# Kernel optimization log

Hardware: AMD Instinct MI355X
Metric: run time of the kernel (lower is better)

The kernel has to match this reference:

```python
import jax, jax.numpy as jnp
import numpy as np

D_STATE = 16; D_MODEL = 256; N_HEADS = 8; N_LAYERS = 4; D_REL = 64
HEALTH = 0
WORLD = (1024.0, 1024.0)
B, T, N = 32, 512, 8
ACTION_DIM = 12


def setup_inputs() -> dict:
    key = jax.random.key(0)
    ks = iter(jax.random.split(key, 48))
    s = 0.02
    def w(shape):
        return jax.random.normal(next(ks), shape, jnp.float32) * s
    inp = dict(
        state=jax.random.normal(next(ks), (B, T, N, D_STATE), jnp.float32),
        pos=jax.random.uniform(next(ks), (B, T, N, 2), jnp.float32),
        vel=jax.random.normal(next(ks), (B, T, N, 2), jnp.float32),
        team_ids=jax.random.randint(next(ks), (B, T, N), 0, 2, jnp.int32),
        alive=jax.random.randint(next(ks), (B, T, N), 0, 2, jnp.int32).astype(bool),
        dead=jnp.zeros((D_STATE,), jnp.float32),
        enc_W1=w((D_STATE, D_MODEL)), enc_b1=jnp.zeros((D_MODEL,), jnp.float32),
        enc_W2=w((D_MODEL, D_MODEL)), enc_b2=jnp.zeros((D_MODEL,), jnp.float32),
        team_emb=w((2, D_MODEL)), ship_emb=w((8, D_MODEL)),
        trunk_W1=w((6, D_REL)), trunk_b1=jnp.zeros((D_REL,), jnp.float32),
        trunk_W2=w((D_REL, D_REL)), trunk_b2=jnp.zeros((D_REL,), jnp.float32),
        adapt_W=w((N_LAYERS, D_REL, N_HEADS)), adapt_b=jnp.zeros((N_LAYERS, N_HEADS), jnp.float32),
        norm_w=jnp.ones((N_LAYERS, D_MODEL), jnp.float32),
        Wq=w((N_LAYERS, D_MODEL, D_MODEL)), bq=jnp.zeros((N_LAYERS, D_MODEL), jnp.float32),
        Wk=w((N_LAYERS, D_MODEL, D_MODEL)), bk=jnp.zeros((N_LAYERS, D_MODEL), jnp.float32),
        Wv=w((N_LAYERS, D_MODEL, D_MODEL)), bv=jnp.zeros((N_LAYERS, D_MODEL), jnp.float32),
        Wo=w((N_LAYERS, D_MODEL, D_MODEL)), bo=jnp.zeros((N_LAYERS, D_MODEL), jnp.float32),
        head_W=w((D_MODEL, ACTION_DIM)), head_b=jnp.zeros((ACTION_DIM,), jnp.float32),
    )
    return inp


def _rms(x, g, eps=1e-6):
    return x * jax.lax.rsqrt(jnp.mean(x * x, axis=-1, keepdims=True) + eps) * g


def reference(state, pos, vel, team_ids, alive, dead,
              enc_W1, enc_b1, enc_W2, enc_b2, team_emb, ship_emb,
              trunk_W1, trunk_b1, trunk_W2, trunk_b2, adapt_W, adapt_b,
              norm_w, Wq, bq, Wk, bk, Wv, bv, Wo, bo, head_W, head_b):
    ws = jnp.asarray(WORLD, state.dtype)
    # replace dead entities' state with learned 'dead' vector
    state = jnp.where(alive[..., None], state, dead)
    # state encoder (MLP)
    h = jax.nn.silu(state @ enc_W1 + enc_b1) @ enc_W2 + enc_b2
    # special embeddings
    h = h + team_emb[team_ids] + ship_emb[jnp.arange(N)]  # ship_emb broadcasts over B,T
    # relational trunk: pairwise toroidal geometry features [B,T,N,N,6]
    p = pos * ws
    rel = p[:, :, :, None, :] - p[:, :, None, :, :]
    rel = rel - jnp.round(rel / ws) * ws  # toroidal wrap
    relv = vel[:, :, :, None, :] - vel[:, :, None, :, :]
    dn = jnp.sqrt(jnp.sum(rel * rel, axis=-1) + 1e-8) / ws[0]
    feats = jnp.concatenate([rel / ws, relv, dn[..., None], 1.0 / (1.0 + dn[..., None])], axis=-1)
    trunk = jax.nn.silu(feats @ trunk_W1 + trunk_b1) @ trunk_W2 + trunk_b2  # [B,T,N,N,D_REL]
    dh = D_MODEL // N_HEADS
    scale = dh ** -0.5
    kmask = alive[:, :, None, None, :]  # mask keys
    x = h
    for i in range(N_LAYERS):
        nx = _rms(x, norm_w[i])
        # adapter: per-layer relational bias [B,T,H,N,N]
        bias = jnp.transpose(trunk @ adapt_W[i] + adapt_b[i], (0, 1, 4, 2, 3))
        q = (nx @ Wq[i] + bq[i]).reshape(B, T, N, N_HEADS, dh)
        k = (nx @ Wk[i] + bk[i]).reshape(B, T, N, N_HEADS, dh)
        v = (nx @ Wv[i] + bv[i]).reshape(B, T, N, N_HEADS, dh)
        sc = jnp.einsum('btihd,btjhd->bthij', q, k) * scale + bias
        sc = jnp.where(kmask, sc, -1e9)
        a = jax.nn.softmax(sc, axis=-1)
        o = jnp.einsum('bthij,btjhd->btihd', a, v).reshape(B, T, N, D_MODEL)
        x = x + o @ Wo[i] + bo[i]
    action_logits = x @ head_W + head_b  # [B,T,N,12]
    return action_logits
```

## Files before the change

kernel.cpp:

```cpp
#include <hip/hip_runtime.h>
#include <cstdint>

#define DEV __device__ __forceinline__

typedef __attribute__((ext_vector_type(8))) short short8;
typedef __attribute__((ext_vector_type(4))) float floatx4;
typedef unsigned short u16;
typedef unsigned int u32;

DEV u16 f2bf(float f) {
    unsigned u = __float_as_uint(f);
    return (u16)((u + 0x7fffu + ((u >> 16) & 1u)) >> 16);
}
DEV void unpack2(u32 u, float& a, float& b) {
    a = __uint_as_float(u << 16);
    b = __uint_as_float(u & 0xffff0000u);
}
DEV u32 pack2f(float a, float b) { return (u32)f2bf(a) | ((u32)f2bf(b) << 16); }
DEV float sigm(float x) { return 1.0f / (1.0f + __expf(-x)); }

#define NAG 8
#define DM 256
#define NL 4
#define AD 12
#define MROWS 32
#define NBLK 4096

#define OFF_E1   0
#define OFF_E2   8192
#define OFF_QKVO 73728
#define OFF_TW2  1122304
#define OFF_ADW  1126400
#define WS_TOTAL 1128448
#define WS_BYTES (WS_TOTAL * 2)

#define L_R1    0
#define L_KB    16896
#define L_V     33792
#define L_R2    50688
#define L_RED   67584
#define L_SPOS  68096
#define L_SVEL  68352
#define SMEM_BYTES 68608

#define TRK(row, col) ((row) * 64 + ((((col) >> 3) ^ ((row) & 7)) << 3) + ((col) & 7))

enum { I_STATE=0, I_POS, I_VEL, I_TEAM, I_ALIVE, I_DEAD, I_EW1, I_EB1, I_EW2, I_EB2,
       I_TEMB, I_SEMB, I_TW1, I_TB1, I_TW2, I_TB2, I_ADW, I_ADB, I_NORMW,
       I_WQ, I_BQ, I_WK, I_BK, I_WV, I_BV, I_WO, I_BO, I_HW, I_HB, N_IN };

struct Args { const void* in[N_IN]; float* out; };

__global__ __launch_bounds__(256) void prep_kernel(Args a, u16* ws)
{
    int e = blockIdx.x * 256 + threadIdx.x;
    int mat = blockIdx.y;
    int size, offs, N, Kreal;
    const float* src;
    if (mat == 0)      { size = 8192;  offs = OFF_E1;  N = 256; Kreal = 16;  src = (const float*)a.in[I_EW1]; }
    else if (mat == 1) { size = 65536; offs = OFF_E2;  N = 256; Kreal = 256; src = (const float*)a.in[I_EW2]; }
    else if (mat < 18) {
        int q = mat - 2, l = q >> 2, m = q & 3;
        int wi = (m == 0) ? I_WQ : (m == 1) ? I_WK : (m == 2) ? I_WV : I_WO;
        size = 65536; offs = OFF_QKVO + q * 65536; N = 256; Kreal = 256;
        src = (const float*)a.in[wi] + l * 65536;
    }
    else if (mat == 18) { size = 4096; offs = OFF_TW2; N = 64; Kreal = 64; src = (const float*)a.in[I_TW2]; }
    else                { size = 2048; offs = OFF_ADW; N = 32; Kreal = 64; src = (const float*)a.in[I_ADW]; }
    if (e >= size) return;
    int ksblk = N * 32;
    int ks = e / ksblk, rem = e % ksblk;
    int n = rem >> 5, quad = (rem >> 3) & 3, j = rem & 7;
    int k = ks * 32 + quad * 8 + j;
    float v = 0.0f;
    if (k < Kreal) {
        if (mat == 19) v = src[((n >> 3) * 64 + k) * 8 + (n & 7)];
        else           v = src[k * N + n];
    }
    ws[offs + e] = f2bf(v);
}

DEV short8 ld_u4(const u16* p) {
    return __builtin_bit_cast(short8, *(const uint4*)p);
}
DEV short8 ld_afrag(const u16* A, int stride, int row0, int kofs, int l15, int quad) {
    return ld_u4(A + (row0 + l15) * stride + kofs + quad * 8);
}
DEV short8 ld_bws(const u16* w, int ksblk, int ks, int col, int l15, int quad) {
    return ld_u4(w + ks * ksblk + (col + l15) * 32 + quad * 8);
}
DEV short8 ld_bf32(const float* W, int N, int Kreal, int ks, int col, int l15, int quad) {
    short8 r;
    #pragma unroll
    for (int j = 0; j < 8; j++) {
        int k = ks * 32 + quad * 8 + j;
        float v = (k < Kreal) ? W[k * N + col + l15] : 0.0f;
        r[j] = (short)f2bf(v);
    }
    return r;
}

template<bool UW>
DEV void gemm32(const u16* A, const u16* wsW, const float* Wf,
                int Kb, int Kreal, int colw, int l15, int quad, floatx4 acc[2][4]) {
    for (int ks = 0; ks < Kb; ks++) {
        short8 af0 = ld_afrag(A, 264, 0,  ks * 32, l15, quad);
        short8 af1 = ld_afrag(A, 264, 16, ks * 32, l15, quad);
        short8 bf[4];
        #pragma unroll
        for (int nj = 0; nj < 4; nj++)
            bf[nj] = UW ? ld_bws(wsW, 8192, ks, colw + nj * 16, l15, quad)
                        : ld_bf32(Wf, 256, Kreal, ks, colw + nj * 16, l15, quad);
        #pragma unroll
        for (int nj = 0; nj < 4; nj++) {
            acc[0][nj] = __builtin_amdgcn_mfma_f32_16x16x32_bf16(af0, bf[nj], acc[0][nj], 0, 0, 0);
            acc[1][nj] = __builtin_amdgcn_mfma_f32_16x16x32_bf16(af1, bf[nj], acc[1][nj], 0, 0, 0);
        }
    }
}

template<bool UW>
__global__ __launch_bounds__(256, 2) void yemong_mfma(Args a, const u16* ws)
{
    extern __shared__ char smem[];
    u16* sR1   = (u16*)(smem + L_R1);
    u16* skb   = (u16*)(smem + L_KB);
    u16* sV    = (u16*)(smem + L_V);
    u16* sR2   = (u16*)(smem + L_R2);
    float* sred = (float*)(smem + L_RED);
    float* spos = (float*)(smem + L_SPOS);
    float* svel = (float*)(smem + L_SVEL);

    const int t = threadIdx.x, bid = blockIdx.x;
    const int lane = t & 63, w = t >> 6;
    const int l15 = lane & 15, quad = lane >> 4;
    const int colw = w * 64;
    const int p = w >> 1, h0 = (w & 1) * 4;

    float xr[2][4][4];
    u32 br[NL][4][2];
    u32 amask;

    unsigned mp = 0;
    const unsigned* au = (const unsigned*)a.in[I_ALIVE];
    #pragma unroll
    for (int i = 0; i < 16; i++) mp |= au[i];
    const bool abyte = (mp > 1u);
    auto aliveAt = [&](int r) -> int {
        int gi = bid * MROWS + r;
        return abyte ? (int)((const unsigned char*)a.in[I_ALIVE])[gi]
                     : ((const int*)a.in[I_ALIVE])[gi];
    };
    auto rms_partials = [&]() {
        float ssv[8];
        #pragma unroll
        for (int mi = 0; mi < 2; mi++)
            #pragma unroll
            for (int r = 0; r < 4; r++) {
                float s = 0.0f;
                #pragma unroll
                for (int nj = 0; nj < 4; nj++) { float v = xr[mi][nj][r]; s = fmaf(v, v, s); }
                ssv[mi * 4 + r] = s;
            }
        #pragma unroll
        for (int m = 1; m < 16; m <<= 1)
            #pragma unroll
            for (int k2 = 0; k2 < 8; k2++) ssv[k2] += __shfl_xor(ssv[k2], m);
        if (l15 == 0) {
            #pragma unroll
            for (int mi = 0; mi < 2; mi++)
                #pragma unroll
                for (int r = 0; r < 4; r++)
                    sred[(mi * 16 + quad * 4 + r) * 4 + w] = ssv[mi * 4 + r];
        }
    };

    if (t < 64) {
        int n = t >> 1, d = t & 1;
        spos[n * 2 + d] = ((const float*)a.in[I_POS])[(bid * MROWS + n) * 2 + d] * 1024.0f;
        svel[n * 2 + d] = ((const float*)a.in[I_VEL])[(bid * MROWS + n) * 2 + d];
    }
    {
        int tk = 2 * p + (quad >> 1);
        amask = 0;
        #pragma unroll
        for (int j = 0; j < 8; j++) amask |= (aliveAt(tk * 8 + j) ? 1u : 0u) << j;
    }
    {
        const float* gs = (const float*)a.in[I_STATE];
        const float* gd = (const float*)a.in[I_DEAD];
        #pragma unroll
        for (int it = 0; it < 4; it++) {
            int idx = t + 256 * it;
            int r = idx >> 5, kk = idx & 31;
            float v = 0.0f;
            if (kk < 16) v = aliveAt(r) ? gs[(bid * MROWS + r) * 16 + kk] : gd[kk];
            sR2[r * 264 + kk] = f2bf(v);
        }
    }
    __syncthreads();

    {
        floatx4 acc[2][4] = {};
        gemm32<UW>(sR2, ws + OFF_E1, (const float*)a.in[I_EW1], 1, 16, colw, l15, quad, acc);
        __syncthreads();
        const float* b1 = (const float*)a.in[I_EB1];
        #pragma unroll
        for (int nj = 0; nj < 4; nj++) {
            int c = colw + nj * 16 + l15;
            float bb = b1[c];
            #pragma unroll
            for (int mi = 0; mi < 2; mi++)
                #pragma unroll
                for (int r = 0; r < 4; r++) {
                    float v = acc[mi][nj][r] + bb;
                    sR2[(mi * 16 + quad * 4 + r) * 264 + c] = f2bf(v * sigm(v));
                }
        }
    }
    __syncthreads();

    {
        floatx4 acc[2][4] = {};
        gemm32<UW>(sR2, ws + OFF_E2, (const float*)a.in[I_EW2], 8, 256, colw, l15, quad, acc);
        const float* b2 = (const float*)a.in[I_EB2];
        const float* te = (const float*)a.in[I_TEMB];
        const float* se = (const float*)a.in[I_SEMB];
        const int* gteam = (const int*)a.in[I_TEAM];
        int team8[8];
        #pragma unroll
        for (int mi = 0; mi < 2; mi++)
            #pragma unroll
            for (int r = 0; r < 4; r++)
                team8[mi * 4 + r] = gteam[bid * MROWS + mi * 16 + quad * 4 + r];
        #pragma unroll
        for (int nj = 0; nj < 4; nj++) {
            int c = colw + nj * 16 + l15;
            float bb = b2[c];
            #pragma unroll
            for (int mi = 0; mi < 2; mi++)
                #pragma unroll
                for (int r = 0; r < 4; r++) {
                    int row = mi * 16 + quad * 4 + r;
                    xr[mi][nj][r] = acc[mi][nj][r] + bb + te[team8[mi * 4 + r] * 256 + c] + se[(row & 7) * 256 + c];
                }
        }
        rms_partials();
    }

    {
        int tokp = t >> 6;
        int pi = tokp * 8 + ((t >> 3) & 7), pj = tokp * 8 + (t & 7);
        float rx = spos[pi * 2 + 0] - spos[pj * 2 + 0];
        float ry = spos[pi * 2 + 1] - spos[pj * 2 + 1];
        rx -= rintf(rx * (1.0f / 1024.0f)) * 1024.0f;
        ry -= rintf(ry * (1.0f / 1024.0f)) * 1024.0f;
        float vx = svel[pi * 2 + 0] - svel[pj * 2 + 0];
        float vy = svel[pi * 2 + 1] - svel[pj * 2 + 1];
        float dn = sqrtf(rx * rx + ry * ry + 1e-8f) * (1.0f / 1024.0f);
        float f[6] = {rx * (1.0f / 1024.0f), ry * (1.0f / 1024.0f), vx, vy, dn, 1.0f / (1.0f + dn)};
        const float* W1 = (const float*)a.in[I_TW1];
        const float* B1 = (const float*)a.in[I_TB1];
        #pragma unroll
        for (int g = 0; g < 8; g++) {
            float v[8];
            #pragma unroll
            for (int e = 0; e < 8; e++) v[e] = B1[g * 8 + e];
            #pragma unroll
            for (int kk = 0; kk < 6; kk++)
                #pragma unroll
                for (int e = 0; e < 8; e++) v[e] = fmaf(f[kk], W1[kk * 64 + g * 8 + e], v[e]);
            #pragma unroll
            for (int e = 0; e < 8; e++) v[e] = v[e] * sigm(v[e]);
            uint4 pk;
            pk.x = pack2f(v[0], v[1]); pk.y = pack2f(v[2], v[3]);
            pk.z = pack2f(v[4], v[5]); pk.w = pack2f(v[6], v[7]);
            *(uint4*)&sR1[t * 64 + ((g ^ (t & 7)) << 3)] = pk;
        }
    }
    __syncthreads();

    {
        short8 taf[4][2];
        #pragma unroll
        for (int mi = 0; mi < 4; mi++)
            #pragma unroll
            for (int ks = 0; ks < 2; ks++) {
                int R = colw + mi * 16 + l15;
                taf[mi][ks] = ld_u4(&sR1[R * 64 + (((ks * 4 + quad) ^ (R & 7)) << 3)]);
            }
        floatx4 tacc[4][4] = {};
        #pragma unroll
        for (int ks = 0; ks < 2; ks++) {
            short8 bf[4];
            #pragma unroll
            for (int nj = 0; nj < 4; nj++)
                bf[nj] = UW ? ld_bws(ws + OFF_TW2, 2048, ks, nj * 16, l15, quad)
                            : ld_bf32((const float*)a.in[I_TW2], 64, 64, ks, nj * 16, l15, quad);
            #pragma unroll
            for (int mi = 0; mi < 4; mi++)
                #pragma unroll
                for (int nj = 0; nj < 4; nj++)
                    tacc[mi][nj] = __builtin_amdgcn_mfma_f32_16x16x32_bf16(taf[mi][ks], bf[nj], tacc[mi][nj], 0, 0, 0);
        }
        const float* B2 = (const float*)a.in[I_TB2];
        #pragma unroll
        for (int nj = 0; nj < 4; nj++) {
            int c = nj * 16 + l15;
            float bb = B2[c];
            #pragma unroll
            for (int mi = 0; mi < 4; mi++)
                #pragma unroll
                for (int r = 0; r < 4; r++) {
                    int row = colw + mi * 16 + quad * 4 + r;
                    sR1[TRK(row, c)] = f2bf(tacc[mi][nj][r] + bb);
                }
        }
    }
    __syncthreads();

    {
        floatx4 tacc[4][2] = {};
        #pragma unroll
        for (int ks = 0; ks < 2; ks++) {
            short8 bf[2];
            #pragma unroll
            for (int nj = 0; nj < 2; nj++) {
                if (UW) bf[nj] = ld_bws(ws + OFF_ADW, 1024, ks, nj * 16, l15, quad);
                else {
                    const float* adw = (const float*)a.in[I_ADW];
                    int n = nj * 16 + l15;
                    #pragma unroll
                    for (int j = 0; j < 8; j++) {
                        int k = ks * 32 + quad * 8 + j;
                        bf[nj][j] = (short)f2bf(k < 64 ? adw[((n >> 3) * 64 + k) * 8 + (n & 7)] : 0.0f);
                    }
                }
            }
            #pragma unroll
            for (int mi = 0; mi < 4; mi++) {
                int R = colw + mi * 16 + l15;
                short8 af = ld_u4(&sR1[R * 64 + (((ks * 4 + quad) ^ (R & 7)) << 3)]);
                #pragma unroll
                for (int nj = 0; nj < 2; nj++)
                    tacc[mi][nj] = __builtin_amdgcn_mfma_f32_16x16x32_bf16(af, bf[nj], tacc[mi][nj], 0, 0, 0);
            }
        }
        const float* adb = (const float*)a.in[I_ADB];
        #pragma unroll
        for (int nj = 0; nj < 2; nj++) {
            int n = nj * 16 + l15;
            float bb = adb[n];
            #pragma unroll
            for (int mi = 0; mi < 4; mi++)
                #pragma unroll
                for (int r = 0; r < 4; r++) {
                    int pl = mi * 16 + quad * 4 + r;
                    sR2[((w * 4 + (n >> 3)) * 8 + (n & 7)) * 64 + pl] = f2bf(tacc[mi][nj][r] + bb);
                }
        }
        __syncthreads();
        int tk = 2 * p + (quad >> 1);
        #pragma unroll
        for (int l = 0; l < NL; l++)
            #pragma unroll
            for (int u = 0; u < 4; u++) {
                int base = ((tk * 4 + l) * 8 + (h0 + u)) * 64 + (l15 & 7) * 8 + (quad & 1) * 4;
                const u32* bp = (const u32*)&sR2[base];
                br[l][u][0] = bp[0];
                br[l][u][1] = bp[1];
            }
    }
    __syncthreads();

    const float* normw = (const float*)a.in[I_NORMW];
    const bool qvalid = ((quad >> 1) == (l15 >> 3));
    #pragma unroll
    for (int l = 0; l < NL; l++) {
        {
            float invr[8];
            #pragma unroll
            for (int mi = 0; mi < 2; mi++)
                #pragma unroll
                for (int r = 0; r < 4; r++) {
                    int row = mi * 16 + quad * 4 + r;
                    float s = sred[row * 4 + 0] + sred[row * 4 + 1] + sred[row * 4 + 2] + sred[row * 4 + 3];
                    invr[mi * 4 + r] = rsqrtf(s * (1.0f / 256.0f) + 1e-6f);
                }
            #pragma unroll
            for (int nj = 0; nj < 4; nj++) {
                int c = colw + nj * 16 + l15;
                float nwv = normw[l * 256 + c];
                #pragma unroll
                for (int mi = 0; mi < 2; mi++)
                    #pragma unroll
                    for (int r = 0; r < 4; r++)
                        sR2[(mi * 16 + quad * 4 + r) * 264 + c] = f2bf(xr[mi][nj][r] * invr[mi * 4 + r] * nwv);
            }
        }
        __syncthreads();

        {
            floatx4 acc[3][2][4] = {};
            const u16* wq  = ws + OFF_QKVO + (l * 4 + 0) * 65536;
            const u16* wk  = ws + OFF_QKVO + (l * 4 + 1) * 65536;
            const u16* wvv = ws + OFF_QKVO + (l * 4 + 2) * 65536;
            const float* fq = (const float*)a.in[I_WQ] + l * 65536;
            const float* fk = (const float*)a.in[I_WK] + l * 65536;
            const float* fv = (const float*)a.in[I_WV] + l * 65536;
            #pragma unroll 2
            for (int ks = 0; ks < 8; ks++) {
                short8 af0 = ld_afrag(sR2, 264, 0,  ks * 32, l15, quad);
                short8 af1 = ld_afrag(sR2, 264, 16, ks * 32, l15, quad);
                short8 bq[4], bk[4], bv[4];
                #pragma unroll
                for (int nj = 0; nj < 4; nj++) {
                    int c = colw + nj * 16;
                    bq[nj] = UW ? ld_bws(wq,  8192, ks, c, l15, quad) : ld_bf32(fq, 256, 256, ks, c, l15, quad);
                    bk[nj] = UW ? ld_bws(wk,  8192, ks, c, l15, quad) : ld_bf32(fk, 256, 256, ks, c, l15, quad);
                    bv[nj] = UW ? ld_bws(wvv, 8192, ks, c, l15, quad) : ld_bf32(fv, 256, 256, ks, c, l15, quad);
                }
                #pragma unroll
                for (int nj = 0; nj < 4; nj++) {
                    acc[0][0][nj] = __builtin_amdgcn_mfma_f32_16x16x32_bf16(af0, bq[nj], acc[0][0][nj], 0, 0, 0);
                    acc[0][1][nj] = __builtin_amdgcn_mfma_f32_16x16x32_bf16(af1, bq[nj], acc[0][1][nj], 0, 0, 0);
                    acc[1][0][nj] = __builtin_amdgcn_mfma_f32_16x16x32_bf16(af0, bk[nj], acc[1][0][nj], 0, 0, 0);
                    acc[1][1][nj] = __builtin_amdgcn_mfma_f32_16x16x32_bf16(af1, bk[nj], acc[1][1][nj], 0, 0, 0);
                    acc[2][0][nj] = __builtin_amdgcn_mfma_f32_16x16x32_bf16(af0, bv[nj], acc[2][0][nj], 0, 0, 0);
                    acc[2][1][nj] = __builtin_amdgcn_mfma_f32_16x16x32_bf16(af1, bv[nj], acc[2][1][nj], 0, 0, 0);
                }
            }
            const float* bqf = (const float*)a.in[I_BQ] + l * 256;
            const float* bkf = (const float*)a.in[I_BK] + l * 256;
            const float* bvf = (const float*)a.in[I_BV] + l * 256;
            #pragma unroll
            for (int nj = 0; nj < 4; nj++) {
                int c = colw + nj * 16 + l15;
                float b0 = bqf[c], b1 = bkf[c], b2v = bvf[c];
                #pragma unroll
                for (int mi = 0; mi < 2; mi++)
                    #pragma unroll
                    for (int r = 0; r < 4; r++) {
                        int row = mi * 16 + quad * 4 + r;
                        sR1[row * 264 + c] = f2bf((acc[0][mi][nj][r] + b0) * 0.17677669529663689f);
                        skb[row * 264 + c] = f2bf(acc[1][mi][nj][r] + b1);
                        sV [row * 264 + c] = f2bf(acc[2][mi][nj][r] + b2v);
                    }
            }
        }
        __syncthreads();

        {
            short8 kf[4], qf[4];
            #pragma unroll
            for (int u = 0; u < 4; u++) {
                int h = h0 + u;
                kf[u] = ld_u4(&skb[(p * 16 + l15) * 264 + h * 32 + quad * 8]);
                qf[u] = ld_u4(&sR1[(p * 16 + l15) * 264 + h * 32 + quad * 8]);
            }
            floatx4 st[4];
            #pragma unroll
            for (int u = 0; u < 4; u++) {
                floatx4 zero = {};
                st[u] = __builtin_amdgcn_mfma_f32_16x16x32_bf16(kf[u], qf[u], zero, 0, 0, 0);
            }
            short8 paf[4];
            #pragma unroll
            for (int u = 0; u < 4; u++) {
                float bb[4];
                unpack2(br[l][u][0], bb[0], bb[1]);
                unpack2(br[l][u][1], bb[2], bb[3]);
                float s[4];
                #pragma unroll
                for (int r = 0; r < 4; r++) {
                    int jl = (quad & 1) * 4 + r;
                    bool alv = (amask >> jl) & 1;
                    s[r] = qvalid ? (alv ? st[u][r] + bb[r] : -1.0e9f) : -2.0e9f;
                }
                float mx = fmaxf(fmaxf(s[0], s[1]), fmaxf(s[2], s[3]));
                mx = fmaxf(mx, __shfl_xor(mx, 16));
                mx = fmaxf(mx, __shfl_xor(mx, 32));
                float e[4], sm = 0.0f;
                #pragma unroll
                for (int r = 0; r < 4; r++) { e[r] = __expf(s[r] - mx); sm += e[r]; }
                sm += __shfl_xor(sm, 16);
                sm += __shfl_xor(sm, 32);
                float inv = 1.0f / sm;
                u32 u01 = pack2f(e[0] * inv, e[1] * inv);
                u32 u23 = pack2f(e[2] * inv, e[3] * inv);
                int srcA = (quad * 32 + l15) & 63;
                u32 a0 = (u32)__shfl((int)u01, srcA);
                u32 a1 = (u32)__shfl((int)u23, srcA);
                u32 a2 = (u32)__shfl((int)u01, (srcA + 16) & 63);
                u32 a3 = (u32)__shfl((int)u23, (srcA + 16) & 63);
                if (quad >= 2) { a0 = 0; a1 = 0; a2 = 0; a3 = 0; }
                uint4 tmp; tmp.x = a0; tmp.y = a1; tmp.z = a2; tmp.w = a3;
                paf[u] = __builtin_bit_cast(short8, tmp);
            }
            #pragma unroll
            for (int u = 0; u < 4; u++) {
                int h = h0 + u;
                #pragma unroll
                for (int nt = 0; nt < 2; nt++) {
                    short8 vf;
                    if (quad < 2) {
                        #pragma unroll
                        for (int jj = 0; jj < 8; jj++) {
                            int kr = quad * 8 + jj;
                            vf[jj] = (short)sV[(p * 16 + kr) * 264 + h * 32 + nt * 16 + l15];
                        }
                    } else {
                        #pragma unroll
                        for (int jj = 0; jj < 8; jj++) vf[jj] = 0;
                    }
                    floatx4 z2 = {};
                    floatx4 o = __builtin_amdgcn_mfma_f32_16x16x32_bf16(paf[u], vf, z2, 0, 0, 0);
                    #pragma unroll
                    for (int r = 0; r < 4; r++)
                        sR1[(p * 16 + quad * 4 + r) * 264 + h * 32 + nt * 16 + l15] = f2bf(o[r]);
                }
            }
        }
        __syncthreads();

        {
            floatx4 acc[2][4] = {};
            gemm32<UW>(sR1, ws + OFF_QKVO + (l * 4 + 3) * 65536, (const float*)a.in[I_WO] + l * 65536,
                       8, 256, colw, l15, quad, acc);
            const float* bo = (const float*)a.in[I_BO] + l * 256;
            #pragma unroll
            for (int nj = 0; nj < 4; nj++) {
                float bb = bo[colw + nj * 16 + l15];
                #pragma unroll
                for (int mi = 0; mi < 2; mi++)
                    #pragma unroll
                    for (int r = 0; r < 4; r++)
                        xr[mi][nj][r] += acc[mi][nj][r] + bb;
            }
            rms_partials();
        }
        __syncthreads();
    }

    {
        float* xf = (float*)sR1;
        #pragma unroll
        for (int nj = 0; nj < 4; nj++) {
            int c = colw + nj * 16 + l15;
            #pragma unroll
            for (int mi = 0; mi < 2; mi++)
                #pragma unroll
                for (int r = 0; r < 4; r++)
                    xf[(mi * 16 + quad * 4 + r) * 264 + c] = xr[mi][nj][r];
        }
        __syncthreads();
        int row = t >> 3, pp = t & 7;
        const float* HW = (const float*)a.in[I_HW];
        float ah[12];
        #pragma unroll
        for (int c = 0; c < 12; c++) ah[c] = 0.0f;
        for (int kk = pp * 32; kk < pp * 32 + 32; kk++) {
            float xv = xf[row * 264 + kk];
            #pragma unroll
            for (int c = 0; c < 12; c++) ah[c] = fmaf(xv, HW[kk * 12 + c], ah[c]);
        }
        #pragma unroll
        for (int c = 0; c < 12; c++) {
            ah[c] += __shfl_xor(ah[c], 1);
            ah[c] += __shfl_xor(ah[c], 2);
            ah[c] += __shfl_xor(ah[c], 4);
        }
        if (pp == 0) {
            const float* hb = (const float*)a.in[I_HB];
            #pragma unroll
            for (int c = 0; c < 12; c++)
                a.out[(bid * MROWS + row) * AD + c] = ah[c] + hb[c];
        }
    }
}

extern "C" void kernel_launch(void* const* d_in, const int* in_sizes, int n_in,
                              void* d_out, int out_size, void* d_ws, size_t ws_size,
                              hipStream_t stream) {
    (void)in_sizes; (void)n_in; (void)out_size;
    Args a;
    for (int i = 0; i < N_IN; i++) a.in[i] = d_in[i];
    a.out = (float*)d_out;
    u16* ws16 = (u16*)d_ws;
    const bool use_ws = (ws_size >= (size_t)WS_BYTES) && (d_ws != nullptr);
    if (use_ws) {
        hipLaunchKernelGGL(prep_kernel, dim3(256, 20), dim3(256), 0, stream, a, ws16);
        hipFuncSetAttribute((const void*)yemong_mfma<true>, hipFuncAttributeMaxDynamicSharedMemorySize, SMEM_BYTES);
        hipLaunchKernelGGL((yemong_mfma<true>), dim3(NBLK), dim3(256), SMEM_BYTES, stream, a, ws16);
    } else {
        hipFuncSetAttribute((const void*)yemong_mfma<false>, hipFuncAttributeMaxDynamicSharedMemorySize, SMEM_BYTES);
        hipLaunchKernelGGL((yemong_mfma<false>), dim3(NBLK), dim3(256), SMEM_BYTES, stream, a, ws16);
    }
}
```

Baseline: 1.124 ms.

## Double rows per block to 64 with 512 threads and reshape GEMM warp tiling

```diff
diff --git a/kernel.cpp b/kernel.cpp
--- a/kernel.cpp
+++ b/kernel.cpp
@@ -23,8 +23,9 @@
 #define DM 256
 #define NL 4
 #define AD 12
-#define MROWS 32
-#define NBLK 4096
+#define MROWS 64
+#define NBLK 2048
+#define THREADS 512
 
 #define OFF_E1   0
 #define OFF_E2   8192
@@ -35,13 +36,13 @@
 #define WS_BYTES (WS_TOTAL * 2)
 
 #define L_R1    0
-#define L_KB    16896
-#define L_V     33792
-#define L_R2    50688
-#define L_RED   67584
-#define L_SPOS  68096
-#define L_SVEL  68352
-#define SMEM_BYTES 68608
+#define L_KB    33792
+#define L_V     67584
+#define L_R2    101376
+#define L_RED   135168
+#define L_SPOS  137216
+#define L_SVEL  137728
+#define SMEM_BYTES 138240
 
 #define TRK(row, col) ((row) * 64 + ((((col) >> 3) ^ ((row) & 7)) << 3) + ((col) & 7))
 
@@ -101,26 +102,29 @@
 }
 
 template<bool UW>
-DEV void gemm32(const u16* A, const u16* wsW, const float* Wf,
-                int Kb, int Kreal, int colw, int l15, int quad, floatx4 acc[2][4]) {
+DEV void gemm64(const u16* A, const u16* wsW, const float* Wf,
+                int Kb, int Kreal, int colw, int l15, int quad, floatx4 acc[4][2]) {
+    #pragma unroll 2
     for (int ks = 0; ks < Kb; ks++) {
-        short8 af0 = ld_afrag(A, 264, 0,  ks * 32, l15, quad);
-        short8 af1 = ld_afrag(A, 264, 16, ks * 32, l15, quad);
-        short8 bf[4];
-        #pragma unroll
-        for (int nj = 0; nj < 4; nj++)
+        short8 af[4];
+        #pragma unroll
+        for (int mi = 0; mi < 4; mi++)
+            af[mi] = ld_afrag(A, 264, mi * 16, ks * 32, l15, quad);
+        short8 bf[2];
+        #pragma unroll
+        for (int nj = 0; nj < 2; nj++)
             bf[nj] = UW ? ld_bws(wsW, 8192, ks, colw + nj * 16, l15, quad)
                         : ld_bf32(Wf, 256, Kreal, ks, colw + nj * 16, l15, quad);
         #pragma unroll
-        for (int nj = 0; nj < 4; nj++) {
-            acc[0][nj] = __builtin_amdgcn_mfma_f32_16x16x32_bf16(af0, bf[nj], acc[0][nj], 0, 0, 0);
-            acc[1][nj] = __builtin_amdgcn_mfma_f32_16x16x32_bf16(af1, bf[nj], acc[1][nj], 0, 0, 0);
-        }
+        for (int mi = 0; mi < 4; mi++)
+            #pragma unroll
+            for (int nj = 0; nj < 2; nj++)
+                acc[mi][nj] = __builtin_amdgcn_mfma_f32_16x16x32_bf16(af[mi], bf[nj], acc[mi][nj], 0, 0, 0);
     }
 }
 
 template<bool UW>
-__global__ __launch_bounds__(256, 2) void yemong_mfma(Args a, const u16* ws)
+__global__ __launch_bounds__(THREADS, 2) void yemong_mfma(Args a, const u16* ws)
 {
     extern __shared__ char smem[];
     u16* sR1   = (u16*)(smem + L_R1);
@@ -134,10 +138,11 @@
     const int t = threadIdx.x, bid = blockIdx.x;
     const int lane = t & 63, w = t >> 6;
     const int l15 = lane & 15, quad = lane >> 4;
-    const int colw = w * 64;
+    const int colw = w * 32;
+    const int rowt = w * 64;
     const int p = w >> 1, h0 = (w & 1) * 4;
 
-    float xr[2][4][4];
+    float xr[4][2][4];
     u32 br[NL][4][2];
     u32 amask;
 
@@ -152,30 +157,28 @@
                      : ((const int*)a.in[I_ALIVE])[gi];
     };
     auto rms_partials = [&]() {
-        float ssv[8];
-        #pragma unroll
-        for (int mi = 0; mi < 2; mi++)
+        float ssv[16];
+        #pragma unroll
+        for (int mi = 0; mi < 4; mi++)
             #pragma unroll
             for (int r = 0; r < 4; r++) {
-                float s = 0.0f;
-                #pragma unroll
-                for (int nj = 0; nj < 4; nj++) { float v = xr[mi][nj][r]; s = fmaf(v, v, s); }
-                ssv[mi * 4 + r] = s;
+                float x0 = xr[mi][0][r], x1 = xr[mi][1][r];
+                ssv[mi * 4 + r] = fmaf(x0, x0, x1 * x1);
             }
         #pragma unroll
         for (int m = 1; m < 16; m <<= 1)
             #pragma unroll
-            for (int k2 = 0; k2 < 8; k2++) ssv[k2] += __shfl_xor(ssv[k2], m);
+            for (int k2 = 0; k2 < 16; k2++) ssv[k2] += __shfl_xor(ssv[k2], m);
         if (l15 == 0) {
             #pragma unroll
-            for (int mi = 0; mi < 2; mi++)
+            for (int mi = 0; mi < 4; mi++)
                 #pragma unroll
                 for (int r = 0; r < 4; r++)
-                    sred[(mi * 16 + quad * 4 + r) * 4 + w] = ssv[mi * 4 + r];
+                    sred[(mi * 16 + quad * 4 + r) * 8 + w] = ssv[mi * 4 + r];
         }
     };
 
-    if (t < 64) {
+    if (t < 128) {
         int n = t >> 1, d = t & 1;
         spos[n * 2 + d] = ((const float*)a.in[I_POS])[(bid * MROWS + n) * 2 + d] * 1024.0f;
         svel[n * 2 + d] = ((const float*)a.in[I_VEL])[(bid * MROWS + n) * 2 + d];
@@ -191,7 +194,7 @@
         const float* gd = (const float*)a.in[I_DEAD];
         #pragma unroll
         for (int it = 0; it < 4; it++) {
-            int idx = t + 256 * it;
+            int idx = t + THREADS * it;
             int r = idx >> 5, kk = idx & 31;
             float v = 0.0f;
             if (kk < 16) v = aliveAt(r) ? gs[(bid * MROWS + r) * 16 + kk] : gd[kk];
@@ -201,16 +204,16 @@
     __syncthreads();
 
     {
-        floatx4 acc[2][4] = {};
-        gemm32<UW>(sR2, ws + OFF_E1, (const float*)a.in[I_EW1], 1, 16, colw, l15, quad, acc);
+        floatx4 acc[4][2] = {};
+        gemm64<UW>(sR2, ws + OFF_E1, (const float*)a.in[I_EW1], 1, 16, colw, l15, quad, acc);
         __syncthreads();
         const float* b1 = (const float*)a.in[I_EB1];
         #pragma unroll
-        for (int nj = 0; nj < 4; nj++) {
+        for (int nj = 0; nj < 2; nj++) {
             int c = colw + nj * 16 + l15;
             float bb = b1[c];
             #pragma unroll
-            for (int mi = 0; mi < 2; mi++)
+            for (int mi = 0; mi < 4; mi++)
                 #pragma unroll
                 for (int r = 0; r < 4; r++) {
                     float v = acc[mi][nj][r] + bb;
@@ -221,28 +224,28 @@
     __syncthreads();
 
     {
-        floatx4 acc[2][4] = {};
-        gemm32<UW>(sR2, ws + OFF_E2, (const float*)a.in[I_EW2], 8, 256, colw, l15, quad, acc);
+        floatx4 acc[4][2] = {};
+        gemm64<UW>(sR2, ws + OFF_E2, (const float*)a.in[I_EW2], 8, 256, colw, l15, quad, acc);
         const float* b2 = (const float*)a.in[I_EB2];
         const float* te = (const float*)a.in[I_TEMB];
         const float* se = (const float*)a.in[I_SEMB];
         const int* gteam = (const int*)a.in[I_TEAM];
-        int team8[8];
-        #pragma unroll
-        for (int mi = 0; mi < 2; mi++)
+        int team16[16];
+        #pragma unroll
+        for (int mi = 0; mi < 4; mi++)
             #pragma unroll
             for (int r = 0; r < 4; r++)
-                team8[mi * 4 + r] = gteam[bid * MROWS + mi * 16 + quad * 4 + r];
-        #pragma unroll
-        for (int nj = 0; nj < 4; nj++) {
+                team16[mi * 4 + r] = gteam[bid * MROWS + mi * 16 + quad * 4 + r];
+        #pragma unroll
+        for (int nj = 0; nj < 2; nj++) {
             int c = colw + nj * 16 + l15;
             float bb = b2[c];
             #pragma unroll
-            for (int mi = 0; mi < 2; mi++)
+            for (int mi = 0; mi < 4; mi++)
                 #pragma unroll
                 for (int r = 0; r < 4; r++) {
                     int row = mi * 16 + quad * 4 + r;
-                    xr[mi][nj][r] = acc[mi][nj][r] + bb + te[team8[mi * 4 + r] * 256 + c] + se[(row & 7) * 256 + c];
+                    xr[mi][nj][r] = acc[mi][nj][r] + bb + te[team16[mi * 4 + r] * 256 + c] + se[(row & 7) * 256 + c];
                 }
         }
         rms_partials();
@@ -286,7 +289,7 @@
         for (int mi = 0; mi < 4; mi++)
             #pragma unroll
             for (int ks = 0; ks < 2; ks++) {
-                int R = colw + mi * 16 + l15;
+                int R = rowt + mi * 16 + l15;
                 taf[mi][ks] = ld_u4(&sR1[R * 64 + (((ks * 4 + quad) ^ (R & 7)) << 3)]);
             }
         floatx4 tacc[4][4] = {};
@@ -312,7 +315,7 @@
             for (int mi = 0; mi < 4; mi++)
                 #pragma unroll
                 for (int r = 0; r < 4; r++) {
-                    int row = colw + mi * 16 + quad * 4 + r;
+                    int row = rowt + mi * 16 + quad * 4 + r;
                     sR1[TRK(row, c)] = f2bf(tacc[mi][nj][r] + bb);
                 }
         }
@@ -339,7 +342,7 @@
             }
             #pragma unroll
             for (int mi = 0; mi < 4; mi++) {
-                int R = colw + mi * 16 + l15;
+                int R = rowt + mi * 16 + l15;
                 short8 af = ld_u4(&sR1[R * 64 + (((ks * 4 + quad) ^ (R & 7)) << 3)]);
                 #pragma unroll
                 for (int nj = 0; nj < 2; nj++)
@@ -378,21 +381,23 @@
     #pragma unroll
     for (int l = 0; l < NL; l++) {
         {
-            float invr[8];
-            #pragma unroll
-            for (int mi = 0; mi < 2; mi++)
+            float invr[16];
+            #pragma unroll
+            for (int mi = 0; mi < 4; mi++)
                 #pragma unroll
                 for (int r = 0; r < 4; r++) {
                     int row = mi * 16 + quad * 4 + r;
-                    float s = sred[row * 4 + 0] + sred[row * 4 + 1] + sred[row * 4 + 2] + sred[row * 4 + 3];
+                    float4 pa = *(const float4*)&sred[row * 8];
+                    float4 pb = *(const float4*)&sred[row * 8 + 4];
+                    float s = pa.x + pa.y + pa.z + pa.w + pb.x + pb.y + pb.z + pb.w;
                     invr[mi * 4 + r] = rsqrtf(s * (1.0f / 256.0f) + 1e-6f);
                 }
             #pragma unroll
-            for (int nj = 0; nj < 4; nj++) {
+            for (int nj = 0; nj < 2; nj++) {
                 int c = colw + nj * 16 + l15;
                 float nwv = normw[l * 256 + c];
                 #pragma unroll
-                for (int mi = 0; mi < 2; mi++)
+                for (int mi = 0; mi < 4; mi++)
                     #pragma unroll
                     for (int r = 0; r < 4; r++)
                         sR2[(mi * 16 + quad * 4 + r) * 264 + c] = f2bf(xr[mi][nj][r] * invr[mi * 4 + r] * nwv);
@@ -401,51 +406,50 @@
         __syncthreads();
 
         {
-            floatx4 acc[3][2][4] = {};
-            const u16* wq  = ws + OFF_QKVO + (l * 4 + 0) * 65536;
-            const u16* wk  = ws + OFF_QKVO + (l * 4 + 1) * 65536;
-            const u16* wvv = ws + OFF_QKVO + (l * 4 + 2) * 65536;
-            const float* fq = (const float*)a.in[I_WQ] + l * 65536;
-            const float* fk = (const float*)a.in[I_WK] + l * 65536;
-            const float* fv = (const float*)a.in[I_WV] + l * 65536;
-            #pragma unroll 2
-            for (int ks = 0; ks < 8; ks++) {
-                short8 af0 = ld_afrag(sR2, 264, 0,  ks * 32, l15, quad);
-                short8 af1 = ld_afrag(sR2, 264, 16, ks * 32, l15, quad);
-                short8 bq[4], bk[4], bv[4];
-                #pragma unroll
-                for (int nj = 0; nj < 4; nj++) {
-                    int c = colw + nj * 16;
-                    bq[nj] = UW ? ld_bws(wq,  8192, ks, c, l15, quad) : ld_bf32(fq, 256, 256, ks, c, l15, quad);
-                    bk[nj] = UW ? ld_bws(wk,  8192, ks, c, l15, quad) : ld_bf32(fk, 256, 256, ks, c, l15, quad);
-                    bv[nj] = UW ? ld_bws(wvv, 8192, ks, c, l15, quad) : ld_bf32(fv, 256, 256, ks, c, l15, quad);
-                }
-                #pragma unroll
-                for (int nj = 0; nj < 4; nj++) {
-                    acc[0][0][nj] = __builtin_amdgcn_mfma_f32_16x16x32_bf16(af0, bq[nj], acc[0][0][nj], 0, 0, 0);
-                    acc[0][1][nj] = __builtin_amdgcn_mfma_f32_16x16x32_bf16(af1, bq[nj], acc[0][1][nj], 0, 0, 0);
-                    acc[1][0][nj] = __builtin_amdgcn_mfma_f32_16x16x32_bf16(af0, bk[nj], acc[1][0][nj], 0, 0, 0);
-                    acc[1][1][nj] = __builtin_amdgcn_mfma_f32_16x16x32_bf16(af1, bk[nj], acc[1][1][nj], 0, 0, 0);
-                    acc[2][0][nj] = __builtin_amdgcn_mfma_f32_16x16x32_bf16(af0, bv[nj], acc[2][0][nj], 0, 0, 0);
-                    acc[2][1][nj] = __builtin_amdgcn_mfma_f32_16x16x32_bf16(af1, bv[nj], acc[2][1][nj], 0, 0, 0);
-                }
-            }
             const float* bqf = (const float*)a.in[I_BQ] + l * 256;
             const float* bkf = (const float*)a.in[I_BK] + l * 256;
             const float* bvf = (const float*)a.in[I_BV] + l * 256;
-            #pragma unroll
-            for (int nj = 0; nj < 4; nj++) {
-                int c = colw + nj * 16 + l15;
-                float b0 = bqf[c], b1 = bkf[c], b2v = bvf[c];
-                #pragma unroll
-                for (int mi = 0; mi < 2; mi++)
+            {
+                floatx4 acc[4][2] = {};
+                gemm64<UW>(sR2, ws + OFF_QKVO + (l * 4 + 0) * 65536, (const float*)a.in[I_WQ] + l * 65536, 8, 256, colw, l15, quad, acc);
+                #pragma unroll
+                for (int nj = 0; nj < 2; nj++) {
+                    int c = colw + nj * 16 + l15;
+                    float bb = bqf[c];
                     #pragma unroll
-                    for (int r = 0; r < 4; r++) {
-                        int row = mi * 16 + quad * 4 + r;
-                        sR1[row * 264 + c] = f2bf((acc[0][mi][nj][r] + b0) * 0.17677669529663689f);
-                        skb[row * 264 + c] = f2bf(acc[1][mi][nj][r] + b1);
-                        sV [row * 264 + c] = f2bf(acc[2][mi][nj][r] + b2v);
-                    }
+                    for (int mi = 0; mi < 4; mi++)
+                        #pragma unroll
+                        for (int r = 0; r < 4; r++)
+                            sR1[(mi * 16 + quad * 4 + r) * 264 + c] = f2bf((acc[mi][nj][r] + bb) * 0.17677669529663689f);
+                }
+            }
+            {
+                floatx4 acc[4][2] = {};
+                gemm64<UW>(sR2, ws + OFF_QKVO + (l * 4 + 1) * 65536, (const float*)a.in[I_WK] + l * 65536, 8, 256, colw, l15, quad, acc);
+                #pragma unroll
+                for (int nj = 0; nj < 2; nj++) {
+                    int c = colw + nj * 16 + l15;
+                    float bb = bkf[c];
+                    #pragma unroll
+                    for (int mi = 0; mi < 4; mi++)
+                        #pragma unroll
+                        for (int r = 0; r < 4; r++)
+                            skb[(mi * 16 + quad * 4 + r) * 264 + c] = f2bf(acc[mi][nj][r] + bb);
+                }
+            }
+            {
+                floatx4 acc[4][2] = {};
+                gemm64<UW>(sR2, ws + OFF_QKVO + (l * 4 + 2) * 65536, (const float*)a.in[I_WV] + l * 65536, 8, 256, colw, l15, quad, acc);
+                #pragma unroll
+                for (int nj = 0; nj < 2; nj++) {
+                    int c = colw + nj * 16 + l15;
+                    float bb = bvf[c];
+                    #pragma unroll
+                    for (int mi = 0; mi < 4; mi++)
+                        #pragma unroll
+                        for (int r = 0; r < 4; r++)
+                            sV[(mi * 16 + quad * 4 + r) * 264 + c] = f2bf(acc[mi][nj][r] + bb);
+                }
             }
         }
         __syncthreads();
@@ -524,15 +528,15 @@
         __syncthreads();
 
         {
-            floatx4 acc[2][4] = {};
-            gemm32<UW>(sR1, ws + OFF_QKVO + (l * 4 + 3) * 65536, (const float*)a.in[I_WO] + l * 65536,
+            floatx4 acc[4][2] = {};
+            gemm64<UW>(sR1, ws + OFF_QKVO + (l * 4 + 3) * 65536, (const float*)a.in[I_WO] + l * 65536,
                        8, 256, colw, l15, quad, acc);
             const float* bo = (const float*)a.in[I_BO] + l * 256;
             #pragma unroll
-            for (int nj = 0; nj < 4; nj++) {
+            for (int nj = 0; nj < 2; nj++) {
                 float bb = bo[colw + nj * 16 + l15];
                 #pragma unroll
-                for (int mi = 0; mi < 2; mi++)
+                for (int mi = 0; mi < 4; mi++)
                     #pragma unroll
                     for (int r = 0; r < 4; r++)
                         xr[mi][nj][r] += acc[mi][nj][r] + bb;
@@ -545,10 +549,10 @@
     {
         float* xf = (float*)sR1;
         #pragma unroll
-        for (int nj = 0; nj < 4; nj++) {
+        for (int nj = 0; nj < 2; nj++) {
             int c = colw + nj * 16 + l15;
             #pragma unroll
-            for (int mi = 0; mi < 2; mi++)
+            for (int mi = 0; mi < 4; mi++)
                 #pragma unroll
                 for (int r = 0; r < 4; r++)
                     xf[(mi * 16 + quad * 4 + r) * 264 + c] = xr[mi][nj][r];
@@ -591,9 +595,9 @@
     if (use_ws) {
         hipLaunchKernelGGL(prep_kernel, dim3(256, 20), dim3(256), 0, stream, a, ws16);
         hipFuncSetAttribute((const void*)yemong_mfma<true>, hipFuncAttributeMaxDynamicSharedMemorySize, SMEM_BYTES);
-        hipLaunchKernelGGL((yemong_mfma<true>), dim3(NBLK), dim3(256), SMEM_BYTES, stream, a, ws16);
+        hipLaunchKernelGGL((yemong_mfma<true>), dim3(NBLK), dim3(THREADS), SMEM_BYTES, stream, a, ws16);
     } else {
         hipFuncSetAttribute((const void*)yemong_mfma<false>, hipFuncAttributeMaxDynamicSharedMemorySize, SMEM_BYTES);
-        hipLaunchKernelGGL((yemong_mfma<false>), dim3(NBLK), dim3(256), SMEM_BYTES, stream, a, ws16);
-    }
-}
+        hipLaunchKernelGGL((yemong_mfma<false>), dim3(NBLK), dim3(THREADS), SMEM_BYTES, stream, a, ws16);
+    }
+}
```

New measurement: 981.5 us. 12.7% less time.
